# Kernel tuning notes

Measured on AMD Instinct MI355X. Metric: run time of the kernel, lower is better.

## Reference

```python
import jax, jax.numpy as jnp
import numpy as np

N_NODES = 50000
N_EDGES = 800000
D_IN = 512
D_OUT = 256

def setup_inputs() -> dict:
    key = jax.random.key(0)
    k1, k2, k3, k4, k5 = jax.random.split(key, 5)
    return {
        "inputs": jax.random.normal(k1, (N_NODES, D_IN), dtype=jnp.float32),
        "weights": jax.random.uniform(k2, (D_IN, D_OUT), dtype=jnp.float32, minval=-0.1, maxval=0.1),
        "bias": jnp.zeros((D_OUT,), dtype=jnp.float32),
        "edge_vals": jax.random.uniform(k3, (N_EDGES,), dtype=jnp.float32),
        "edge_row": jax.random.randint(k4, (N_EDGES,), 0, N_NODES),
        "edge_col": jax.random.randint(k5, (N_EDGES,), 0, N_NODES),
    }

def reference(inputs, weights, bias, edge_vals, edge_row, edge_col):
    # dense projection: [N, D_in] @ [D_in, D_out] -> [N, D_out]
    supports = inputs @ weights
    # sparse adjacency spmm in COO form: out[i] = sum_e vals[e] * supports[col[e]] for row[e] == i
    msgs = supports[edge_col] * edge_vals[:, None]  # [E, D_out]
    aggregated = jax.ops.segment_sum(msgs, edge_row, num_segments=inputs.shape[0])
    return aggregated + bias
```

## Files before the change

### kernel.cpp

```cpp
#include <hip/hip_runtime.h>

#define D_IN 512
#define D_OUT 256
#define BM 64
#define BN 256
#define BK 32
#define NT (D_IN / BK)

typedef short short8 __attribute__((ext_vector_type(8)));
typedef float floatx4 __attribute__((ext_vector_type(4)));

static __device__ __forceinline__ unsigned short f2bf(float f) {
    unsigned u = __float_as_uint(f);
    u += 0x7FFF + ((u >> 16) & 1);
    return (unsigned short)(u >> 16);
}
static __device__ __forceinline__ float bf2f(unsigned short h) {
    return __uint_as_float((unsigned)h << 16);
}

#define CONV_BLOCKS 256
__global__ __launch_bounds__(512) void convert_and_zero(const float* __restrict__ W,
                                                        unsigned short* __restrict__ Wt,
                                                        int* __restrict__ cnt, int NZ) {
    int b = blockIdx.x;
    if (b < CONV_BLOCKS) {
        int t = b * 512 + threadIdx.x;
        int n = t >> 9;
        int k = t & 511;
        Wt[t] = f2bf(W[(size_t)k * D_OUT + n]);
    } else {
        int i = (b - CONV_BLOCKS) * 512 + threadIdx.x;
        if (i < NZ) cnt[i] = 0;
    }
}

__global__ __launch_bounds__(256) void hist_rows(const int* __restrict__ rows,
                                                 int* __restrict__ cnt, int E) {
    int e0 = (blockIdx.x * 256 + threadIdx.x) * 4;
    if (e0 + 3 < E) {
        int4 r = *(const int4*)(rows + e0);
        atomicAdd(&cnt[r.x], 1);
        atomicAdd(&cnt[r.y], 1);
        atomicAdd(&cnt[r.z], 1);
        atomicAdd(&cnt[r.w], 1);
    } else {
        for (int e = e0; e < E; ++e) atomicAdd(&cnt[rows[e]], 1);
    }
}

#define SCAN_B 4096
#define SCAN_READY (1 << 30)
__global__ __launch_bounds__(1024) void scan_blocks(const int* __restrict__ cnt,
                                                    int* __restrict__ ptr,
                                                    int* __restrict__ partials, int M) {
    __shared__ int wsum[16];
    __shared__ int s_off;
    const int t = threadIdx.x, lane = t & 63, wave = t >> 6;
    const int base = blockIdx.x * SCAN_B + t * 4;
    int4 v = make_int4(0, 0, 0, 0);
    if (base + 3 < M) v = *(const int4*)(cnt + base);
    else {
        if (base + 0 < M) v.x = cnt[base + 0];
        if (base + 1 < M) v.y = cnt[base + 1];
        if (base + 2 < M) v.z = cnt[base + 2];
        if (base + 3 < M) v.w = cnt[base + 3];
    }
    int s = v.x + v.y + v.z + v.w;
    int incl = s;
#pragma unroll
    for (int off = 1; off < 64; off <<= 1) {
        int x = __shfl_up(incl, off, 64);
        if (lane >= off) incl += x;
    }
    if (lane == 63) wsum[wave] = incl;
    __syncthreads();
    if (t == 0) {
        int run = 0;
#pragma unroll
        for (int w = 0; w < 16; ++w) { int x = wsum[w]; wsum[w] = run; run += x; }
        atomicExch(&partials[blockIdx.x], run | SCAN_READY);
        int off = 0;
        for (int j = 0; j < (int)blockIdx.x; ++j) {
            int pv;
            do { pv = atomicAdd(&partials[j], 0); } while (!(pv & SCAN_READY));
            off += pv & ~SCAN_READY;
        }
        s_off = off;
    }
    __syncthreads();
    int g = s_off + wsum[wave] + (incl - s);
    int e0 = g, e1 = e0 + v.x, e2 = e1 + v.y, e3 = e2 + v.z;
    if (base + 3 < M) *(int4*)(ptr + base) = make_int4(e0, e1, e2, e3);
    else {
        if (base + 0 < M) ptr[base + 0] = e0;
        if (base + 1 < M) ptr[base + 1] = e1;
        if (base + 2 < M) ptr[base + 2] = e2;
        if (base + 3 < M) ptr[base + 3] = e3;
    }
}

__global__ __launch_bounds__(512) void gemm_build(
    const float* __restrict__ A, const unsigned short* __restrict__ Wt,
    unsigned short* __restrict__ S, int M, int nGemm,
    const float* __restrict__ vals, const int* __restrict__ rows,
    const int* __restrict__ cols, int* __restrict__ ptr,
    unsigned long long* __restrict__ edges, int E) {
    __shared__ unsigned short As[4 * BM * 8];
    __shared__ unsigned short Bs[4 * BN * 8];
    const int bid = blockIdx.x;
    const int tid = threadIdx.x;

    if (bid >= nGemm) {
        int e0 = (bid - nGemm) * 2048 + tid * 4;
        if (e0 + 3 < E) {
            int4   rr = *(const int4*)(rows + e0);
            int4   cc = *(const int4*)(cols + e0);
            float4 vv = *(const float4*)(vals + e0);
            int p0 = atomicAdd(&ptr[rr.x], 1);
            __builtin_nontemporal_store(
                (unsigned long long)(unsigned)cc.x |
                ((unsigned long long)(unsigned)__float_as_int(vv.x) << 32), edges + p0);
            int p1 = atomicAdd(&ptr[rr.y], 1);
            __builtin_nontemporal_store(
                (unsigned long long)(unsigned)cc.y |
                ((unsigned long long)(unsigned)__float_as_int(vv.y) << 32), edges + p1);
            int p2 = atomicAdd(&ptr[rr.z], 1);
            __builtin_nontemporal_store(
                (unsigned long long)(unsigned)cc.z |
                ((unsigned long long)(unsigned)__float_as_int(vv.z) << 32), edges + p2);
            int p3 = atomicAdd(&ptr[rr.w], 1);
            __builtin_nontemporal_store(
                (unsigned long long)(unsigned)cc.w |
                ((unsigned long long)(unsigned)__float_as_int(vv.w) << 32), edges + p3);
        } else {
            for (int e = e0; e < E; ++e) {
                int pos = atomicAdd(&ptr[rows[e]], 1);
                unsigned long long packed =
                    (unsigned long long)(unsigned)cols[e] |
                    ((unsigned long long)(unsigned)__float_as_int(vals[e]) << 32);
                __builtin_nontemporal_store(packed, edges + pos);
            }
        }
        return;
    }

    const int bm   = bid * BM;
    const int lane = tid & 63;
    const int wave = tid >> 6;
    const int l15  = lane & 15;
    const int quad = lane >> 4;
    const int wn   = wave * 32;

    const bool isA  = tid < 256;
    const int  arow = tid & 63;
    const int  apl  = (tid >> 6) & 3;
    const bool aval = isA && (bm + arow) < M;
    const float* aptr = A + (size_t)(aval ? bm + arow : 0) * D_IN + apl * 8;
    const int awoff = (apl * BM + arow) * 8;

    const int brow = tid & 255;
    const int bp0  = tid >> 8;
    const unsigned short* bptr0 = Wt + (size_t)brow * D_IN + bp0 * 8;
    const unsigned short* bptr1 = Wt + (size_t)brow * D_IN + (bp0 + 2) * 8;
    const int bwoff0 = (bp0 * BN + brow) * 8;
    const int bwoff1 = ((bp0 + 2) * BN + brow) * 8;

    float4 a0lo, a0hi, a1lo, a1hi;
    short8 b0r0, b0r1, b1r0, b1r1;
    const float4 fz = make_float4(0.f, 0.f, 0.f, 0.f);
    a0lo = aval ? *(const float4*)(aptr + 0) : fz;
    a0hi = aval ? *(const float4*)(aptr + 4) : fz;
    b0r0 = *(const short8*)(bptr0 + 0);
    b0r1 = *(const short8*)(bptr1 + 0);
    a1lo = aval ? *(const float4*)(aptr + BK) : fz;
    a1hi = aval ? *(const float4*)(aptr + BK + 4) : fz;
    b1r0 = *(const short8*)(bptr0 + BK);
    b1r1 = *(const short8*)(bptr1 + BK);

    floatx4 acc[4][2] = {};

#define GEMM_STEP(T, ALO, AHI, BR0, BR1)                                          \
    {                                                                             \
        if (isA) {                                                                \
            short8 a8;                                                            \
            a8[0] = (short)f2bf(ALO.x); a8[1] = (short)f2bf(ALO.y);               \
            a8[2] = (short)f2bf(ALO.z); a8[3] = (short)f2bf(ALO.w);               \
            a8[4] = (short)f2bf(AHI.x); a8[5] = (short)f2bf(AHI.y);               \
            a8[6] = (short)f2bf(AHI.z); a8[7] = (short)f2bf(AHI.w);               \
            *(short8*)(As + awoff) = a8;                                          \
        }                                                                         \
        *(short8*)(Bs + bwoff0) = BR0;                                            \
        *(short8*)(Bs + bwoff1) = BR1;                                            \
        __syncthreads();                                                          \
        if ((T) + 2 < NT) {                                                       \
            int ko = ((T) + 2) * BK;                                              \
            ALO = aval ? *(const float4*)(aptr + ko) : fz;                        \
            AHI = aval ? *(const float4*)(aptr + ko + 4) : fz;                    \
            BR0 = *(const short8*)(bptr0 + ko);                                   \
            BR1 = *(const short8*)(bptr1 + ko);                                   \
        }                                                                         \
        short8 af[4], bfr[2];                                                     \
        _Pragma("unroll")                                                         \
        for (int i = 0; i < 4; ++i)                                               \
            af[i] = *(const short8*)(As + (quad * BM + i * 16 + l15) * 8);        \
        _Pragma("unroll")                                                         \
        for (int j = 0; j < 2; ++j)                                               \
            bfr[j] = *(const short8*)(Bs + (quad * BN + wn + j * 16 + l15) * 8);  \
        _Pragma("unroll")                                                         \
        for (int i = 0; i < 4; ++i)                                               \
            _Pragma("unroll")                                                     \
            for (int j = 0; j < 2; ++j)                                           \
                acc[i][j] = __builtin_amdgcn_mfma_f32_16x16x32_bf16(              \
                    af[i], bfr[j], acc[i][j], 0, 0, 0);                           \
        __syncthreads();                                                          \
    }

#pragma unroll
    for (int t2 = 0; t2 < NT; t2 += 2) {
        GEMM_STEP(t2,     a0lo, a0hi, b0r0, b0r1);
        GEMM_STEP(t2 + 1, a1lo, a1hi, b1r0, b1r1);
    }
#undef GEMM_STEP

#pragma unroll
    for (int i = 0; i < 4; ++i) {
#pragma unroll
        for (int r = 0; r < 4; ++r) {
            int gm = bm + i * 16 + quad * 4 + r;
            if (gm < M) {
#pragma unroll
                for (int j = 0; j < 2; ++j)
                    S[(size_t)gm * D_OUT + wn + j * 16 + l15] = f2bf(acc[i][j][r]);
            }
        }
    }
}

__global__ __launch_bounds__(256) void spmm_rows(const unsigned short* __restrict__ S,
                                                 const int2* __restrict__ edges,
                                                 const int* __restrict__ ptr,
                                                 const float* __restrict__ bias,
                                                 float* __restrict__ out, int M) {
    const int row = blockIdx.x * 4 + (threadIdx.x >> 6);
    if (row >= M) return;
    const int lane = threadIdx.x & 63;
    float4 a0 = ((const float4*)bias)[lane];
    float4 a1 = make_float4(0.f, 0.f, 0.f, 0.f);
    const int beg = row ? ptr[row - 1] : 0;
    const int end = ptr[row];
    int j = beg;
    for (; j + 7 < end; j += 8) {
        int2 e0 = edges[j + 0], e1 = edges[j + 1], e2 = edges[j + 2], e3 = edges[j + 3];
        int2 e4 = edges[j + 4], e5 = edges[j + 5], e6 = edges[j + 6], e7 = edges[j + 7];
        ushort4 s0 = ((const ushort4*)(S + (size_t)e0.x * D_OUT))[lane];
        ushort4 s1 = ((const ushort4*)(S + (size_t)e1.x * D_OUT))[lane];
        ushort4 s2 = ((const ushort4*)(S + (size_t)e2.x * D_OUT))[lane];
        ushort4 s3 = ((const ushort4*)(S + (size_t)e3.x * D_OUT))[lane];
        ushort4 s4 = ((const ushort4*)(S + (size_t)e4.x * D_OUT))[lane];
        ushort4 s5 = ((const ushort4*)(S + (size_t)e5.x * D_OUT))[lane];
        ushort4 s6 = ((const ushort4*)(S + (size_t)e6.x * D_OUT))[lane];
        ushort4 s7 = ((const ushort4*)(S + (size_t)e7.x * D_OUT))[lane];
        float v0 = __int_as_float(e0.y), v1 = __int_as_float(e1.y);
        float v2 = __int_as_float(e2.y), v3 = __int_as_float(e3.y);
        float v4 = __int_as_float(e4.y), v5 = __int_as_float(e5.y);
        float v6 = __int_as_float(e6.y), v7 = __int_as_float(e7.y);
        a0.x += v0 * bf2f(s0.x) + v2 * bf2f(s2.x) + v4 * bf2f(s4.x) + v6 * bf2f(s6.x);
        a0.y += v0 * bf2f(s0.y) + v2 * bf2f(s2.y) + v4 * bf2f(s4.y) + v6 * bf2f(s6.y);
        a0.z += v0 * bf2f(s0.z) + v2 * bf2f(s2.z) + v4 * bf2f(s4.z) + v6 * bf2f(s6.z);
        a0.w += v0 * bf2f(s0.w) + v2 * bf2f(s2.w) + v4 * bf2f(s4.w) + v6 * bf2f(s6.w);
        a1.x += v1 * bf2f(s1.x) + v3 * bf2f(s3.x) + v5 * bf2f(s5.x) + v7 * bf2f(s7.x);
        a1.y += v1 * bf2f(s1.y) + v3 * bf2f(s3.y) + v5 * bf2f(s5.y) + v7 * bf2f(s7.y);
        a1.z += v1 * bf2f(s1.z) + v3 * bf2f(s3.z) + v5 * bf2f(s5.z) + v7 * bf2f(s7.z);
        a1.w += v1 * bf2f(s1.w) + v3 * bf2f(s3.w) + v5 * bf2f(s5.w) + v7 * bf2f(s7.w);
    }
    for (; j + 3 < end; j += 4) {
        int2 e0 = edges[j], e1 = edges[j + 1], e2 = edges[j + 2], e3 = edges[j + 3];
        ushort4 s0 = ((const ushort4*)(S + (size_t)e0.x * D_OUT))[lane];
        ushort4 s1 = ((const ushort4*)(S + (size_t)e1.x * D_OUT))[lane];
        ushort4 s2 = ((const ushort4*)(S + (size_t)e2.x * D_OUT))[lane];
        ushort4 s3 = ((const ushort4*)(S + (size_t)e3.x * D_OUT))[lane];
        float v0 = __int_as_float(e0.y), v1 = __int_as_float(e1.y);
        float v2 = __int_as_float(e2.y), v3 = __int_as_float(e3.y);
        a0.x += v0 * bf2f(s0.x) + v2 * bf2f(s2.x);
        a0.y += v0 * bf2f(s0.y) + v2 * bf2f(s2.y);
        a0.z += v0 * bf2f(s0.z) + v2 * bf2f(s2.z);
        a0.w += v0 * bf2f(s0.w) + v2 * bf2f(s2.w);
        a1.x += v1 * bf2f(s1.x) + v3 * bf2f(s3.x);
        a1.y += v1 * bf2f(s1.y) + v3 * bf2f(s3.y);
        a1.z += v1 * bf2f(s1.z) + v3 * bf2f(s3.z);
        a1.w += v1 * bf2f(s1.w) + v3 * bf2f(s3.w);
    }
    for (; j < end; ++j) {
        int2 e = edges[j];
        float v = __int_as_float(e.y);
        ushort4 s = ((const ushort4*)(S + (size_t)e.x * D_OUT))[lane];
        a0.x += v * bf2f(s.x);
        a0.y += v * bf2f(s.y);
        a0.z += v * bf2f(s.z);
        a0.w += v * bf2f(s.w);
    }
    a0.x += a1.x; a0.y += a1.y; a0.z += a1.z; a0.w += a1.w;
    floatx4 res = {a0.x, a0.y, a0.z, a0.w};
    __builtin_nontemporal_store(res, (floatx4*)(out + (size_t)row * D_OUT) + lane);
}

extern "C" void kernel_launch(void* const* d_in, const int* in_sizes, int n_in,
                              void* d_out, int out_size, void* d_ws, size_t ws_size,
                              hipStream_t stream) {
    const float* inputs    = (const float*)d_in[0];
    const float* weights   = (const float*)d_in[1];
    const float* bias      = (const float*)d_in[2];
    const float* edge_vals = (const float*)d_in[3];
    const int*   edge_row  = (const int*)d_in[4];
    const int*   edge_col  = (const int*)d_in[5];
    float* out = (float*)d_out;

    const int M = in_sizes[0] / D_IN;
    const int E = in_sizes[3];

    char* ws = (char*)d_ws;
    unsigned short* S  = (unsigned short*)ws;
    unsigned short* Wt = (unsigned short*)(ws + (size_t)M * D_OUT * 2);
    unsigned long long* edges = (unsigned long long*)((char*)Wt + (size_t)D_OUT * D_IN * 2);
    int*  ptr          = (int*)((char*)edges + (size_t)E * 8);
    int*  cnt          = ptr + ((M + 4) & ~3);
    int*  partials     = cnt + M;

    int NZ = M + 16;
    convert_and_zero<<<CONV_BLOCKS + (NZ + 511) / 512, 512, 0, stream>>>(weights, Wt, cnt, NZ);

    hist_rows<<<(E + 1023) / 1024, 256, 0, stream>>>(edge_row, cnt, E);
    scan_blocks<<<(M + SCAN_B - 1) / SCAN_B, 1024, 0, stream>>>(cnt, ptr, partials, M);

    int nGemm  = (M + BM - 1) / BM;
    int nBuild = (E + 2047) / 2048;
    gemm_build<<<nGemm + nBuild, 512, 0, stream>>>(inputs, Wt, S, M, nGemm,
                                                   edge_vals, edge_row, edge_col,
                                                   ptr, edges, E);

    spmm_rows<<<(M + 3) / 4, 256, 0, stream>>>(S, (const int2*)edges, ptr, bias, out, M);
}
```

Baseline: 360.4 us.

## Make GEMM persistent with half of W resident in LDS, fold edge build into a wave

The fused GEMM and edge-build kernel becomes a persistent 128x2 grid. Each block loads half of the bf16 weight matrix (128 output columns) into 128KB of LDS once. Each of eight waves then computes 16-row tiles independently, converting A to bf16 in registers with no block-level syncs. A ninth wave per block scatters a contiguous chunk of edges into CSR order. This removes per-tile W reloads and barriers, but A is now read twice (once per column half), occupancy is low (one large block per CU), edge scatter runs on few waves, and the scalar tail path for edges was dropped.

```diff
diff --git a/kernel.cpp b/kernel.cpp
--- a/kernel.cpp
+++ b/kernel.cpp
@@ -2,10 +2,6 @@
 
 #define D_IN 512
 #define D_OUT 256
-#define BM 64
-#define BN 256
-#define BK 32
-#define NT (D_IN / BK)
 
 typedef short short8 __attribute__((ext_vector_type(8)));
 typedef float floatx4 __attribute__((ext_vector_type(4)));
@@ -100,23 +96,40 @@
     }
 }
 
-__global__ __launch_bounds__(512) void gemm_build(
+__global__ __launch_bounds__(576) void gemm_build(
     const float* __restrict__ A, const unsigned short* __restrict__ Wt,
-    unsigned short* __restrict__ S, int M, int nGemm,
+    unsigned short* __restrict__ S, int M,
     const float* __restrict__ vals, const int* __restrict__ rows,
     const int* __restrict__ cols, int* __restrict__ ptr,
     unsigned long long* __restrict__ edges, int E) {
-    __shared__ unsigned short As[4 * BM * 8];
-    __shared__ unsigned short Bs[4 * BN * 8];
-    const int bid = blockIdx.x;
+    __shared__ unsigned short Bs[64 * 128 * 8];
     const int tid = threadIdx.x;
-
-    if (bid >= nGemm) {
-        int e0 = (bid - nGemm) * 2048 + tid * 4;
-        if (e0 + 3 < E) {
-            int4   rr = *(const int4*)(rows + e0);
-            int4   cc = *(const int4*)(cols + e0);
-            float4 vv = *(const float4*)(vals + e0);
+    const int bx  = blockIdx.x;
+    const int ny  = blockIdx.y;
+
+    const unsigned short* wbase = Wt + (size_t)(ny * 128) * D_IN;
+    for (int c = tid; c < 64 * 128; c += 576) {
+        int p = c >> 7, col = c & 127;
+        *(short8*)(Bs + (size_t)c * 8) =
+            *(const short8*)(wbase + (size_t)col * D_IN + p * 8);
+    }
+    __syncthreads();
+
+    const int wave = tid >> 6;
+    const int lane = tid & 63;
+    const int l15  = lane & 15;
+    const int quad = lane >> 4;
+
+    if (wave == 8) {
+        const int nB  = gridDim.x * gridDim.y;
+        const int b   = ny * gridDim.x + bx;
+        const int per = (((E + nB - 1) / nB) + 3) & ~3;
+        const long base = (long)b * per;
+        int count = (int)(E - base); if (count > per) count = per;
+        for (int e = (int)base + lane * 4; e < base + count; e += 256) {
+            int4   rr = *(const int4*)(rows + e);
+            int4   cc = *(const int4*)(cols + e);
+            float4 vv = *(const float4*)(vals + e);
             int p0 = atomicAdd(&ptr[rr.x], 1);
             __builtin_nontemporal_store(
                 (unsigned long long)(unsigned)cc.x |
@@ -133,105 +146,56 @@
             __builtin_nontemporal_store(
                 (unsigned long long)(unsigned)cc.w |
                 ((unsigned long long)(unsigned)__float_as_int(vv.w) << 32), edges + p3);
-        } else {
-            for (int e = e0; e < E; ++e) {
-                int pos = atomicAdd(&ptr[rows[e]], 1);
-                unsigned long long packed =
-                    (unsigned long long)(unsigned)cols[e] |
-                    ((unsigned long long)(unsigned)__float_as_int(vals[e]) << 32);
-                __builtin_nontemporal_store(packed, edges + pos);
-            }
         }
         return;
     }
 
-    const int bm   = bid * BM;
-    const int lane = tid & 63;
-    const int wave = tid >> 6;
-    const int l15  = lane & 15;
-    const int quad = lane >> 4;
-    const int wn   = wave * 32;
-
-    const bool isA  = tid < 256;
-    const int  arow = tid & 63;
-    const int  apl  = (tid >> 6) & 3;
-    const bool aval = isA && (bm + arow) < M;
-    const float* aptr = A + (size_t)(aval ? bm + arow : 0) * D_IN + apl * 8;
-    const int awoff = (apl * BM + arow) * 8;
-
-    const int brow = tid & 255;
-    const int bp0  = tid >> 8;
-    const unsigned short* bptr0 = Wt + (size_t)brow * D_IN + bp0 * 8;
-    const unsigned short* bptr1 = Wt + (size_t)brow * D_IN + (bp0 + 2) * 8;
-    const int bwoff0 = (bp0 * BN + brow) * 8;
-    const int bwoff1 = ((bp0 + 2) * BN + brow) * 8;
-
-    float4 a0lo, a0hi, a1lo, a1hi;
-    short8 b0r0, b0r1, b1r0, b1r1;
-    const float4 fz = make_float4(0.f, 0.f, 0.f, 0.f);
-    a0lo = aval ? *(const float4*)(aptr + 0) : fz;
-    a0hi = aval ? *(const float4*)(aptr + 4) : fz;
-    b0r0 = *(const short8*)(bptr0 + 0);
-    b0r1 = *(const short8*)(bptr1 + 0);
-    a1lo = aval ? *(const float4*)(aptr + BK) : fz;
-    a1hi = aval ? *(const float4*)(aptr + BK + 4) : fz;
-    b1r0 = *(const short8*)(bptr0 + BK);
-    b1r1 = *(const short8*)(bptr1 + BK);
-
-    floatx4 acc[4][2] = {};
-
-#define GEMM_STEP(T, ALO, AHI, BR0, BR1)                                          \
-    {                                                                             \
-        if (isA) {                                                                \
-            short8 a8;                                                            \
-            a8[0] = (short)f2bf(ALO.x); a8[1] = (short)f2bf(ALO.y);               \
-            a8[2] = (short)f2bf(ALO.z); a8[3] = (short)f2bf(ALO.w);               \
-            a8[4] = (short)f2bf(AHI.x); a8[5] = (short)f2bf(AHI.y);               \
-            a8[6] = (short)f2bf(AHI.z); a8[7] = (short)f2bf(AHI.w);               \
-            *(short8*)(As + awoff) = a8;                                          \
-        }                                                                         \
-        *(short8*)(Bs + bwoff0) = BR0;                                            \
-        *(short8*)(Bs + bwoff1) = BR1;                                            \
-        __syncthreads();                                                          \
-        if ((T) + 2 < NT) {                                                       \
-            int ko = ((T) + 2) * BK;                                              \
-            ALO = aval ? *(const float4*)(aptr + ko) : fz;                        \
-            AHI = aval ? *(const float4*)(aptr + ko + 4) : fz;                    \
-            BR0 = *(const short8*)(bptr0 + ko);                                   \
-            BR1 = *(const short8*)(bptr1 + ko);                                   \
-        }                                                                         \
-        short8 af[4], bfr[2];                                                     \
-        _Pragma("unroll")                                                         \
-        for (int i = 0; i < 4; ++i)                                               \
-            af[i] = *(const short8*)(As + (quad * BM + i * 16 + l15) * 8);        \
-        _Pragma("unroll")                                                         \
-        for (int j = 0; j < 2; ++j)                                               \
-            bfr[j] = *(const short8*)(Bs + (quad * BN + wn + j * 16 + l15) * 8);  \
-        _Pragma("unroll")                                                         \
-        for (int i = 0; i < 4; ++i)                                               \
+    const int nTiles = (M + 15) >> 4;
+    for (int rt = bx * 8 + wave; rt < nTiles; rt += gridDim.x * 8) {
+        const int row0 = rt << 4;
+        int arow = row0 + l15; if (arow >= M) arow = M - 1;
+        const float* ap = A + (size_t)arow * D_IN + quad * 8;
+
+        floatx4 acc[8] = {};
+
+        float4 p0l, p0h, p1l, p1h, p2l, p2h, p3l, p3h;
+        p0l = *(const float4*)(ap + 0);   p0h = *(const float4*)(ap + 4);
+        p1l = *(const float4*)(ap + 32);  p1h = *(const float4*)(ap + 36);
+        p2l = *(const float4*)(ap + 64);  p2h = *(const float4*)(ap + 68);
+        p3l = *(const float4*)(ap + 96);  p3h = *(const float4*)(ap + 100);
+
+#define STEP(T, PL, PH)                                                           \
+        {                                                                         \
+            short8 af;                                                            \
+            af[0] = (short)f2bf(PL.x); af[1] = (short)f2bf(PL.y);                 \
+            af[2] = (short)f2bf(PL.z); af[3] = (short)f2bf(PL.w);                 \
+            af[4] = (short)f2bf(PH.x); af[5] = (short)f2bf(PH.y);                 \
+            af[6] = (short)f2bf(PH.z); af[7] = (short)f2bf(PH.w);                 \
+            if ((T) + 4 < 16) {                                                   \
+                PL = *(const float4*)(ap + ((T) + 4) * 32);                       \
+                PH = *(const float4*)(ap + ((T) + 4) * 32 + 4);                   \
+            }                                                                     \
+            const unsigned short* bb =                                            \
+                Bs + ((size_t)((T) * 4 + quad) * 128 + l15) * 8;                  \
             _Pragma("unroll")                                                     \
-            for (int j = 0; j < 2; ++j)                                           \
-                acc[i][j] = __builtin_amdgcn_mfma_f32_16x16x32_bf16(              \
-                    af[i], bfr[j], acc[i][j], 0, 0, 0);                           \
-        __syncthreads();                                                          \
-    }
+            for (int c = 0; c < 8; ++c)                                           \
+                acc[c] = __builtin_amdgcn_mfma_f32_16x16x32_bf16(                 \
+                    af, *(const short8*)(bb + c * 128), acc[c], 0, 0, 0);         \
+        }
+
+        STEP(0,  p0l, p0h) STEP(1,  p1l, p1h) STEP(2,  p2l, p2h) STEP(3,  p3l, p3h)
+        STEP(4,  p0l, p0h) STEP(5,  p1l, p1h) STEP(6,  p2l, p2h) STEP(7,  p3l, p3h)
+        STEP(8,  p0l, p0h) STEP(9,  p1l, p1h) STEP(10, p2l, p2h) STEP(11, p3l, p3h)
+        STEP(12, p0l, p0h) STEP(13, p1l, p1h) STEP(14, p2l, p2h) STEP(15, p3l, p3h)
+#undef STEP
 
 #pragma unroll
-    for (int t2 = 0; t2 < NT; t2 += 2) {
-        GEMM_STEP(t2,     a0lo, a0hi, b0r0, b0r1);
-        GEMM_STEP(t2 + 1, a1lo, a1hi, b1r0, b1r1);
-    }
-#undef GEMM_STEP
-
+        for (int c = 0; c < 8; ++c) {
 #pragma unroll
-    for (int i = 0; i < 4; ++i) {
-#pragma unroll
-        for (int r = 0; r < 4; ++r) {
-            int gm = bm + i * 16 + quad * 4 + r;
-            if (gm < M) {
-#pragma unroll
-                for (int j = 0; j < 2; ++j)
-                    S[(size_t)gm * D_OUT + wn + j * 16 + l15] = f2bf(acc[i][j][r]);
+            for (int r = 0; r < 4; ++r) {
+                int gm = row0 + quad * 4 + r;
+                if (gm < M)
+                    S[(size_t)gm * D_OUT + ny * 128 + c * 16 + l15] = f2bf(acc[c][r]);
             }
         }
     }
@@ -333,11 +297,9 @@
     hist_rows<<<(E + 1023) / 1024, 256, 0, stream>>>(edge_row, cnt, E);
     scan_blocks<<<(M + SCAN_B - 1) / SCAN_B, 1024, 0, stream>>>(cnt, ptr, partials, M);
 
-    int nGemm  = (M + BM - 1) / BM;
-    int nBuild = (E + 2047) / 2048;
-    gemm_build<<<nGemm + nBuild, 512, 0, stream>>>(inputs, Wt, S, M, nGemm,
-                                                   edge_vals, edge_row, edge_col,
-                                                   ptr, edges, E);
+    gemm_build<<<dim3(128, 2), 576, 0, stream>>>(inputs, Wt, S, M,
+                                                 edge_vals, edge_row, edge_col,
+                                                 ptr, edges, E);
 
     spmm_rows<<<(M + 3) / 4, 256, 0, stream>>>(S, (const int2*)edges, ptr, bias, out, M);
 }
```

New measurement: 560.1 us. +55.4%, slower.

## Fuse histogram and scan kernels with a global completion counter; roll GEMM loop

Applied to the files above, without the earlier changes.

Merges the row histogram and the prefix-scan kernels into one launch. Scan blocks spin on a global counter until every histogram block has finished, which saves a kernel launch and its inter-kernel gap. The GEMM k-loop is also changed from a manually unrolled double-register prefetch to a rolled single-buffer loop, with a launch-bounds occupancy hint of 4 added. Spin-waiting depends on the histogram blocks being scheduled before the scan blocks, and the shorter prefetch distance may expose more global load latency in the GEMM.

```diff
diff --git a/kernel.cpp b/kernel.cpp
--- a/kernel.cpp
+++ b/kernel.cpp
@@ -5,7 +5,6 @@
 #define BM 64
 #define BN 256
 #define BK 32
-#define NT (D_IN / BK)
 
 typedef short short8 __attribute__((ext_vector_type(8)));
 typedef float floatx4 __attribute__((ext_vector_type(4)));
@@ -35,29 +34,45 @@
     }
 }
 
-__global__ __launch_bounds__(256) void hist_rows(const int* __restrict__ rows,
-                                                 int* __restrict__ cnt, int E) {
-    int e0 = (blockIdx.x * 256 + threadIdx.x) * 4;
-    if (e0 + 3 < E) {
-        int4 r = *(const int4*)(rows + e0);
-        atomicAdd(&cnt[r.x], 1);
-        atomicAdd(&cnt[r.y], 1);
-        atomicAdd(&cnt[r.z], 1);
-        atomicAdd(&cnt[r.w], 1);
-    } else {
-        for (int e = e0; e < E; ++e) atomicAdd(&cnt[rows[e]], 1);
-    }
-}
-
 #define SCAN_B 4096
 #define SCAN_READY (1 << 30)
-__global__ __launch_bounds__(1024) void scan_blocks(const int* __restrict__ cnt,
-                                                    int* __restrict__ ptr,
-                                                    int* __restrict__ partials, int M) {
+__global__ __launch_bounds__(1024) void hist_scan(const int* __restrict__ rows,
+                                                  int* __restrict__ cnt,
+                                                  int* __restrict__ ptr,
+                                                  int* __restrict__ partials,
+                                                  int* __restrict__ histdone,
+                                                  int M, int E, int NH) {
+    const int t = threadIdx.x;
+    const int bid = blockIdx.x;
+
+    if (bid < NH) {
+        int e0 = bid * 4096 + t * 4;
+        if (e0 + 3 < E) {
+            int4 r = *(const int4*)(rows + e0);
+            atomicAdd(&cnt[r.x], 1);
+            atomicAdd(&cnt[r.y], 1);
+            atomicAdd(&cnt[r.z], 1);
+            atomicAdd(&cnt[r.w], 1);
+        } else {
+            for (int e = e0; e < E; ++e) atomicAdd(&cnt[rows[e]], 1);
+        }
+        __threadfence();
+        __syncthreads();
+        if (t == 0) atomicAdd(histdone, 1);
+        return;
+    }
+
+    if (t == 0) {
+        while (atomicAdd(histdone, 0) != NH) { }
+    }
+    __syncthreads();
+    __threadfence();
+
     __shared__ int wsum[16];
     __shared__ int s_off;
-    const int t = threadIdx.x, lane = t & 63, wave = t >> 6;
-    const int base = blockIdx.x * SCAN_B + t * 4;
+    const int sb = bid - NH;
+    const int lane = t & 63, wave = t >> 6;
+    const int base = sb * SCAN_B + t * 4;
     int4 v = make_int4(0, 0, 0, 0);
     if (base + 3 < M) v = *(const int4*)(cnt + base);
     else {
@@ -79,9 +94,9 @@
         int run = 0;
 #pragma unroll
         for (int w = 0; w < 16; ++w) { int x = wsum[w]; wsum[w] = run; run += x; }
-        atomicExch(&partials[blockIdx.x], run | SCAN_READY);
+        atomicExch(&partials[sb], run | SCAN_READY);
         int off = 0;
-        for (int j = 0; j < (int)blockIdx.x; ++j) {
+        for (int j = 0; j < sb; ++j) {
             int pv;
             do { pv = atomicAdd(&partials[j], 0); } while (!(pv & SCAN_READY));
             off += pv & ~SCAN_READY;
@@ -100,7 +115,7 @@
     }
 }
 
-__global__ __launch_bounds__(512) void gemm_build(
+__global__ __launch_bounds__(512, 4) void gemm_build(
     const float* __restrict__ A, const unsigned short* __restrict__ Wt,
     unsigned short* __restrict__ S, int M, int nGemm,
     const float* __restrict__ vals, const int* __restrict__ rows,
@@ -166,62 +181,49 @@
     const int bwoff0 = (bp0 * BN + brow) * 8;
     const int bwoff1 = ((bp0 + 2) * BN + brow) * 8;
 
-    float4 a0lo, a0hi, a1lo, a1hi;
-    short8 b0r0, b0r1, b1r0, b1r1;
     const float4 fz = make_float4(0.f, 0.f, 0.f, 0.f);
-    a0lo = aval ? *(const float4*)(aptr + 0) : fz;
-    a0hi = aval ? *(const float4*)(aptr + 4) : fz;
-    b0r0 = *(const short8*)(bptr0 + 0);
-    b0r1 = *(const short8*)(bptr1 + 0);
-    a1lo = aval ? *(const float4*)(aptr + BK) : fz;
-    a1hi = aval ? *(const float4*)(aptr + BK + 4) : fz;
-    b1r0 = *(const short8*)(bptr0 + BK);
-    b1r1 = *(const short8*)(bptr1 + BK);
+    float4 aR0 = aval ? *(const float4*)(aptr + 0) : fz;
+    float4 aR1 = aval ? *(const float4*)(aptr + 4) : fz;
+    short8 bR0 = *(const short8*)bptr0;
+    short8 bR1 = *(const short8*)bptr1;
 
     floatx4 acc[4][2] = {};
 
-#define GEMM_STEP(T, ALO, AHI, BR0, BR1)                                          \
-    {                                                                             \
-        if (isA) {                                                                \
-            short8 a8;                                                            \
-            a8[0] = (short)f2bf(ALO.x); a8[1] = (short)f2bf(ALO.y);               \
-            a8[2] = (short)f2bf(ALO.z); a8[3] = (short)f2bf(ALO.w);               \
-            a8[4] = (short)f2bf(AHI.x); a8[5] = (short)f2bf(AHI.y);               \
-            a8[6] = (short)f2bf(AHI.z); a8[7] = (short)f2bf(AHI.w);               \
-            *(short8*)(As + awoff) = a8;                                          \
-        }                                                                         \
-        *(short8*)(Bs + bwoff0) = BR0;                                            \
-        *(short8*)(Bs + bwoff1) = BR1;                                            \
-        __syncthreads();                                                          \
-        if ((T) + 2 < NT) {                                                       \
-            int ko = ((T) + 2) * BK;                                              \
-            ALO = aval ? *(const float4*)(aptr + ko) : fz;                        \
-            AHI = aval ? *(const float4*)(aptr + ko + 4) : fz;                    \
-            BR0 = *(const short8*)(bptr0 + ko);                                   \
-            BR1 = *(const short8*)(bptr1 + ko);                                   \
-        }                                                                         \
-        short8 af[4], bfr[2];                                                     \
-        _Pragma("unroll")                                                         \
-        for (int i = 0; i < 4; ++i)                                               \
-            af[i] = *(const short8*)(As + (quad * BM + i * 16 + l15) * 8);        \
-        _Pragma("unroll")                                                         \
-        for (int j = 0; j < 2; ++j)                                               \
-            bfr[j] = *(const short8*)(Bs + (quad * BN + wn + j * 16 + l15) * 8);  \
-        _Pragma("unroll")                                                         \
-        for (int i = 0; i < 4; ++i)                                               \
-            _Pragma("unroll")                                                     \
-            for (int j = 0; j < 2; ++j)                                           \
-                acc[i][j] = __builtin_amdgcn_mfma_f32_16x16x32_bf16(              \
-                    af[i], bfr[j], acc[i][j], 0, 0, 0);                           \
-        __syncthreads();                                                          \
-    }
-
-#pragma unroll
-    for (int t2 = 0; t2 < NT; t2 += 2) {
-        GEMM_STEP(t2,     a0lo, a0hi, b0r0, b0r1);
-        GEMM_STEP(t2 + 1, a1lo, a1hi, b1r0, b1r1);
-    }
-#undef GEMM_STEP
+    for (int k0 = 0; k0 < D_IN; k0 += BK) {
+        if (isA) {
+            short8 a8;
+            a8[0] = (short)f2bf(aR0.x); a8[1] = (short)f2bf(aR0.y);
+            a8[2] = (short)f2bf(aR0.z); a8[3] = (short)f2bf(aR0.w);
+            a8[4] = (short)f2bf(aR1.x); a8[5] = (short)f2bf(aR1.y);
+            a8[6] = (short)f2bf(aR1.z); a8[7] = (short)f2bf(aR1.w);
+            *(short8*)(As + awoff) = a8;
+        }
+        *(short8*)(Bs + bwoff0) = bR0;
+        *(short8*)(Bs + bwoff1) = bR1;
+        __syncthreads();
+
+        if (k0 + BK < D_IN) {
+            aR0 = aval ? *(const float4*)(aptr + k0 + BK + 0) : fz;
+            aR1 = aval ? *(const float4*)(aptr + k0 + BK + 4) : fz;
+            bR0 = *(const short8*)(bptr0 + k0 + BK);
+            bR1 = *(const short8*)(bptr1 + k0 + BK);
+        }
+
+        short8 af[4], bfr[2];
+#pragma unroll
+        for (int i = 0; i < 4; ++i)
+            af[i] = *(const short8*)(As + (quad * BM + i * 16 + l15) * 8);
+#pragma unroll
+        for (int j = 0; j < 2; ++j)
+            bfr[j] = *(const short8*)(Bs + (quad * BN + wn + j * 16 + l15) * 8);
+#pragma unroll
+        for (int i = 0; i < 4; ++i)
+#pragma unroll
+            for (int j = 0; j < 2; ++j)
+                acc[i][j] = __builtin_amdgcn_mfma_f32_16x16x32_bf16(
+                    af[i], bfr[j], acc[i][j], 0, 0, 0);
+        __syncthreads();
+    }
 
 #pragma unroll
     for (int i = 0; i < 4; ++i) {
@@ -326,12 +328,15 @@
     int*  ptr          = (int*)((char*)edges + (size_t)E * 8);
     int*  cnt          = ptr + ((M + 4) & ~3);
     int*  partials     = cnt + M;
-
-    int NZ = M + 16;
+    int*  histdone     = partials + 16;
+
+    int NZ = M + 32;
     convert_and_zero<<<CONV_BLOCKS + (NZ + 511) / 512, 512, 0, stream>>>(weights, Wt, cnt, NZ);
 
-    hist_rows<<<(E + 1023) / 1024, 256, 0, stream>>>(edge_row, cnt, E);
-    scan_blocks<<<(M + SCAN_B - 1) / SCAN_B, 1024, 0, stream>>>(cnt, ptr, partials, M);
+    int NH = (E + 4095) / 4096;
+    int NS = (M + SCAN_B - 1) / SCAN_B;
+    hist_scan<<<NH + NS, 1024, 0, stream>>>(edge_row, cnt, ptr, partials, histdone,
+                                            M, E, NH);
 
     int nGemm  = (M + BM - 1) / BM;
     int nBuild = (E + 2047) / 2048;
```

After: 391.1 us. 8.5% more time.
